# Optimization experiments

Hardware: AMD Instinct MI355X
Metric: run time of the kernel (lower is better)

Reference implementation:

```python
import jax, jax.numpy as jnp
import numpy as np

GAMMA = 10.0
EPS = 1e-6  # epsilon from __init__
B, D, C = 128, 1024, 1000


def setup_inputs() -> dict:
    key = jax.random.key(0)
    k1, k2, k3, k4 = jax.random.split(key, 4)
    return {
        "activations": jax.random.normal(k1, (B, D), jnp.float32),
        "W": jax.random.normal(k2, (D, C), jnp.float32) * 0.02,
        "b": jax.random.normal(k3, (C,), jnp.float32) * 0.02,
        "targets": jax.random.randint(k4, (B,), 0, C),
    }


def reference(activations, W, b, targets):
    # Linear classifier head: logits must be a differentiable fn of activations
    def head(a):  # [D] -> [C]
        return a @ W + b

    logits = jax.vmap(head)(activations)          # [B, C]
    # Batched Jacobian replaces the per-(i,j) torch.autograd.grad loop.
    J = jax.vmap(jax.jacrev(head))(activations)   # [B, C, D]

    t1h = jax.nn.one_hot(targets, C, dtype=logits.dtype)       # [B, C]
    correct = jnp.sum(logits * t1h, axis=1)                    # [B]
    grad_correct = jnp.einsum('bcd,bc->bd', J, t1h)            # [B, D]

    grad_diff = J - grad_correct[:, None, :]                   # [B, C, D]
    # dual norm (l2): sqrt(sum sq + eps), then forward adds +eps again
    dual_norm = jnp.sqrt(jnp.sum(grad_diff * grad_diff, axis=2) + EPS) + EPS  # [B, C]

    score_diff = logits - correct[:, None]                     # [B, C]
    violation = jax.nn.relu(GAMMA + score_diff / dual_norm)    # [B, C]
    violation = violation * (1.0 - t1h)  # exclude target class (relu >= 0 so max unaffected)

    loss = jnp.max(violation, axis=1)  # aggregation = 'max' over incorrect classes
    return jnp.mean(loss)
```

## Files before the change

kernel.cpp:

```cpp
#include <hip/hip_runtime.h>
#include <math.h>

#define Bn 128
#define Dn 1024
#define Cn 1000
#define Cpad 1024
#define GAMMA 10.0f
#define EPSv 1e-6f

#define DCH 32
#define DSPAN (Dn / DCH)
#define BM 8
#define NBG (Bn / BM)


__global__ __launch_bounds__(256) void lm_partial(
    const float* __restrict__ A, const float* __restrict__ W,
    const int* __restrict__ tgt,
    float* __restrict__ lg, float* __restrict__ dt,
    float* __restrict__ nrm, float* __restrict__ out)
{
    const int tid = threadIdx.x;
    const int bg  = blockIdx.x;
    const int k   = blockIdx.y;
    if (bg == 0 && k == 0 && tid == 0) out[0] = 0.f;

    const int b0 = bg * BM;
    const int d0 = k * DSPAN;
    const int c0 = tid * 4;
    const bool valid = (c0 < Cn);
    const int c0m = valid ? c0 : 0;

    __shared__ float4 AsI[2][DSPAN];
    __shared__ float4 WtI[2][DSPAN];
    {
        const int i = tid & (DSPAN - 1);
        const int j = tid >> 5;
        ((float*)&AsI[j >> 2][i])[j & 3] = A[(b0 + j) * Dn + d0 + i];
        ((float*)&WtI[j >> 2][i])[j & 3] = W[(size_t)(d0 + i) * Cn + tgt[b0 + j]];
    }
    __syncthreads();

    float aL[BM][4], aD[BM][4], aN[4];
    #pragma unroll
    for (int e = 0; e < 4; ++e) {
        aN[e] = 0.f;
        #pragma unroll
        for (int j = 0; j < BM; ++j) { aL[j][e] = 0.f; aD[j][e] = 0.f; }
    }

    const float* Wp = W + (size_t)d0 * Cn + c0m;
    #pragma unroll 2
    for (int i = 0; i < DSPAN; ++i) {
        const float4 w   = *(const float4*)(Wp + (size_t)i * Cn);
        const float4 a40 = AsI[0][i];
        const float4 a41 = AsI[1][i];
        const float4 t40 = WtI[0][i];
        const float4 t41 = WtI[1][i];
        const float wv[4] = {w.x, w.y, w.z, w.w};
        const float av[8] = {a40.x, a40.y, a40.z, a40.w, a41.x, a41.y, a41.z, a41.w};
        const float tv[8] = {t40.x, t40.y, t40.z, t40.w, t41.x, t41.y, t41.z, t41.w};
        #pragma unroll
        for (int e = 0; e < 4; ++e) {
            aN[e] = fmaf(wv[e], wv[e], aN[e]);
            #pragma unroll
            for (int j = 0; j < BM; ++j) {
                aL[j][e] = fmaf(av[j], wv[e], aL[j][e]);
                aD[j][e] = fmaf(tv[j], wv[e], aD[j][e]);
            }
        }
    }

    if (valid) {
        #pragma unroll
        for (int j = 0; j < BM; ++j) {
            const size_t off = ((size_t)(k * Bn + b0 + j)) * Cpad + c0;
            *(float4*)&lg[off] = make_float4(aL[j][0], aL[j][1], aL[j][2], aL[j][3]);
            *(float4*)&dt[off] = make_float4(aD[j][0], aD[j][1], aD[j][2], aD[j][3]);
        }
        if (bg == 0)
            *(float4*)&nrm[(size_t)k * Cpad + c0] =
                make_float4(aN[0], aN[1], aN[2], aN[3]);
    }
}

__global__ __launch_bounds__(256) void lm_final(
    const float* __restrict__ lg, const float* __restrict__ dt,
    const float* __restrict__ nrm, const float* __restrict__ bias,
    const int* __restrict__ tgt, float* __restrict__ out)
{
    const int b = blockIdx.x;
    const int tid = threadIdx.x;
    const int t = tgt[b];

    __shared__ float s_cr, s_nt;
    if (tid < DCH) {
        float cr = lg[((size_t)(tid * Bn + b)) * Cpad + t];
        float nt = nrm[(size_t)tid * Cpad + t];
        #pragma unroll
        for (int off = 16; off; off >>= 1) {
            cr += __shfl_down(cr, off, 64);
            nt += __shfl_down(nt, off, 64);
        }
        if (tid == 0) { s_cr = cr + bias[t]; s_nt = nt; }
    }
    __syncthreads();

    float m = 0.f;
    if (tid < 250) {
        const int c0 = tid * 4;
        float L[4] = {0.f,0.f,0.f,0.f}, Dt[4] = {0.f,0.f,0.f,0.f}, Nr[4] = {0.f,0.f,0.f,0.f};
        #pragma unroll 8
        for (int k = 0; k < DCH; ++k) {
            const float4 l4 = *(const float4*)&lg[((size_t)(k * Bn + b)) * Cpad + c0];
            const float4 d4 = *(const float4*)&dt[((size_t)(k * Bn + b)) * Cpad + c0];
            const float4 n4 = *(const float4*)&nrm[(size_t)k * Cpad + c0];
            L[0] += l4.x; L[1] += l4.y; L[2] += l4.z; L[3] += l4.w;
            Dt[0] += d4.x; Dt[1] += d4.y; Dt[2] += d4.z; Dt[3] += d4.w;
            Nr[0] += n4.x; Nr[1] += n4.y; Nr[2] += n4.z; Nr[3] += n4.w;
        }
        const float4 bi = *(const float4*)&bias[c0];
        const float bv[4] = {bi.x, bi.y, bi.z, bi.w};
        const float cr = s_cr, nt = s_nt;
        #pragma unroll
        for (int e = 0; e < 4; ++e) {
            const int c = c0 + e;
            if (c != t) {
                float dist = fmaxf(Nr[e] + nt - 2.f * Dt[e], 0.f);
                float dn   = sqrtf(dist + EPSv) + EPSv;
                float v    = GAMMA + (L[e] + bv[e] - cr) / dn;
                m = fmaxf(m, v);
            }
        }
    }

    for (int off = 32; off; off >>= 1) m = fmaxf(m, __shfl_down(m, off, 64));
    __shared__ float sm[4];
    if ((tid & 63) == 0) sm[tid >> 6] = m;
    __syncthreads();
    if (tid == 0) {
        const float bm = fmaxf(fmaxf(sm[0], sm[1]), fmaxf(sm[2], sm[3]));
        atomicAdd(out, bm * (1.0f / (float)Bn));
    }
}

extern "C" void kernel_launch(void* const* d_in, const int* in_sizes, int n_in,
                              void* d_out, int out_size, void* d_ws, size_t ws_size,
                              hipStream_t stream) {
    const float* A    = (const float*)d_in[0];
    const float* W    = (const float*)d_in[1];
    const float* bias = (const float*)d_in[2];
    const int*   tgt  = (const int*)d_in[3];
    float* out = (float*)d_out;

    float* lg  = (float*)d_ws;
    float* dt  = lg + (size_t)DCH * Bn * Cpad;
    float* nrm = dt + (size_t)DCH * Bn * Cpad;

    lm_partial<<<dim3(NBG, DCH), dim3(256), 0, stream>>>(A, W, tgt, lg, dt, nrm, out);
    lm_final<<<dim3(Bn), dim3(256), 0, stream>>>(lg, dt, nrm, bias, tgt, out);
}
```

Measured before the change: 83.98 us.

## Rebalance split-K partial GEMM and split class reduction across blocks

Halves the D-chunk count and the batch rows per block in the partial kernel. The grid stays the same size, but each thread keeps fewer accumulators and each block writes half as many partial sums to workspace. The final reduction is split into four class-quarters per batch row. Per-row maxima are combined with an integer atomicMax on float bits (valid because the values are non-negative), and a third tiny kernel averages them into the output. The cost is an extra kernel launch, and W is re-read with less reuse across batch rows per load.

```diff
diff --git a/kernel.cpp b/kernel.cpp
--- a/kernel.cpp
+++ b/kernel.cpp
@@ -8,9 +8,9 @@
 #define GAMMA 10.0f
 #define EPSv 1e-6f
 
-#define DCH 32
+#define DCH 16
 #define DSPAN (Dn / DCH)
-#define BM 8
+#define BM 4
 #define NBG (Bn / BM)
 
 
@@ -18,12 +18,12 @@
     const float* __restrict__ A, const float* __restrict__ W,
     const int* __restrict__ tgt,
     float* __restrict__ lg, float* __restrict__ dt,
-    float* __restrict__ nrm, float* __restrict__ out)
+    float* __restrict__ nrm, int* __restrict__ vmax)
 {
     const int tid = threadIdx.x;
     const int bg  = blockIdx.x;
     const int k   = blockIdx.y;
-    if (bg == 0 && k == 0 && tid == 0) out[0] = 0.f;
+    if (bg == 0 && k == 0 && tid < Bn) vmax[tid] = 0;
 
     const int b0 = bg * BM;
     const int d0 = k * DSPAN;
@@ -31,13 +31,13 @@
     const bool valid = (c0 < Cn);
     const int c0m = valid ? c0 : 0;
 
-    __shared__ float4 AsI[2][DSPAN];
-    __shared__ float4 WtI[2][DSPAN];
+    __shared__ float4 As4[DSPAN];
+    __shared__ float4 Wt4[DSPAN];
     {
         const int i = tid & (DSPAN - 1);
-        const int j = tid >> 5;
-        ((float*)&AsI[j >> 2][i])[j & 3] = A[(b0 + j) * Dn + d0 + i];
-        ((float*)&WtI[j >> 2][i])[j & 3] = W[(size_t)(d0 + i) * Cn + tgt[b0 + j]];
+        const int j = tid >> 6;
+        ((float*)&As4[i])[j] = A[(b0 + j) * Dn + d0 + i];
+        ((float*)&Wt4[i])[j] = W[(size_t)(d0 + i) * Cn + tgt[b0 + j]];
     }
     __syncthreads();
 
@@ -50,16 +50,14 @@
     }
 
     const float* Wp = W + (size_t)d0 * Cn + c0m;
-    #pragma unroll 2
+    #pragma unroll 4
     for (int i = 0; i < DSPAN; ++i) {
-        const float4 w   = *(const float4*)(Wp + (size_t)i * Cn);
-        const float4 a40 = AsI[0][i];
-        const float4 a41 = AsI[1][i];
-        const float4 t40 = WtI[0][i];
-        const float4 t41 = WtI[1][i];
+        const float4 w  = *(const float4*)(Wp + (size_t)i * Cn);
+        const float4 a4 = As4[i];
+        const float4 t4 = Wt4[i];
         const float wv[4] = {w.x, w.y, w.z, w.w};
-        const float av[8] = {a40.x, a40.y, a40.z, a40.w, a41.x, a41.y, a41.z, a41.w};
-        const float tv[8] = {t40.x, t40.y, t40.z, t40.w, t41.x, t41.y, t41.z, t41.w};
+        const float av[4] = {a4.x, a4.y, a4.z, a4.w};
+        const float tv[4] = {t4.x, t4.y, t4.z, t4.w};
         #pragma unroll
         for (int e = 0; e < 4; ++e) {
             aN[e] = fmaf(wv[e], wv[e], aN[e]);
@@ -84,21 +82,22 @@
     }
 }
 
-__global__ __launch_bounds__(256) void lm_final(
+__global__ __launch_bounds__(256) void lm_vmax(
     const float* __restrict__ lg, const float* __restrict__ dt,
     const float* __restrict__ nrm, const float* __restrict__ bias,
-    const int* __restrict__ tgt, float* __restrict__ out)
+    const int* __restrict__ tgt, int* __restrict__ vmax)
 {
-    const int b = blockIdx.x;
+    const int b   = blockIdx.x;
+    const int q   = blockIdx.y;
     const int tid = threadIdx.x;
-    const int t = tgt[b];
+    const int t   = tgt[b];
 
     __shared__ float s_cr, s_nt;
     if (tid < DCH) {
         float cr = lg[((size_t)(tid * Bn + b)) * Cpad + t];
         float nt = nrm[(size_t)tid * Cpad + t];
         #pragma unroll
-        for (int off = 16; off; off >>= 1) {
+        for (int off = DCH / 2; off; off >>= 1) {
             cr += __shfl_down(cr, off, 64);
             nt += __shfl_down(nt, off, 64);
         }
@@ -108,40 +107,43 @@
 
     float m = 0.f;
     if (tid < 250) {
-        const int c0 = tid * 4;
-        float L[4] = {0.f,0.f,0.f,0.f}, Dt[4] = {0.f,0.f,0.f,0.f}, Nr[4] = {0.f,0.f,0.f,0.f};
-        #pragma unroll 8
+        const int c = q * 250 + tid;
+        float L = 0.f, Dt = 0.f, Nr = 0.f;
+        #pragma unroll
         for (int k = 0; k < DCH; ++k) {
-            const float4 l4 = *(const float4*)&lg[((size_t)(k * Bn + b)) * Cpad + c0];
-            const float4 d4 = *(const float4*)&dt[((size_t)(k * Bn + b)) * Cpad + c0];
-            const float4 n4 = *(const float4*)&nrm[(size_t)k * Cpad + c0];
-            L[0] += l4.x; L[1] += l4.y; L[2] += l4.z; L[3] += l4.w;
-            Dt[0] += d4.x; Dt[1] += d4.y; Dt[2] += d4.z; Dt[3] += d4.w;
-            Nr[0] += n4.x; Nr[1] += n4.y; Nr[2] += n4.z; Nr[3] += n4.w;
+            L  += lg[((size_t)(k * Bn + b)) * Cpad + c];
+            Dt += dt[((size_t)(k * Bn + b)) * Cpad + c];
+            Nr += nrm[(size_t)k * Cpad + c];
         }
-        const float4 bi = *(const float4*)&bias[c0];
-        const float bv[4] = {bi.x, bi.y, bi.z, bi.w};
-        const float cr = s_cr, nt = s_nt;
-        #pragma unroll
-        for (int e = 0; e < 4; ++e) {
-            const int c = c0 + e;
-            if (c != t) {
-                float dist = fmaxf(Nr[e] + nt - 2.f * Dt[e], 0.f);
-                float dn   = sqrtf(dist + EPSv) + EPSv;
-                float v    = GAMMA + (L[e] + bv[e] - cr) / dn;
-                m = fmaxf(m, v);
-            }
+        if (c != t) {
+            const float dist = fmaxf(Nr + s_nt - 2.f * Dt, 0.f);
+            const float dn   = sqrtf(dist + EPSv) + EPSv;
+            m = fmaxf(0.f, GAMMA + (L + bias[c] - s_cr) / dn);
         }
     }
 
+    #pragma unroll
     for (int off = 32; off; off >>= 1) m = fmaxf(m, __shfl_down(m, off, 64));
     __shared__ float sm[4];
     if ((tid & 63) == 0) sm[tid >> 6] = m;
     __syncthreads();
     if (tid == 0) {
         const float bm = fmaxf(fmaxf(sm[0], sm[1]), fmaxf(sm[2], sm[3]));
-        atomicAdd(out, bm * (1.0f / (float)Bn));
+        atomicMax(vmax + b, __float_as_int(bm));
     }
+}
+
+__global__ __launch_bounds__(128) void lm_mean(
+    const int* __restrict__ vmax, float* __restrict__ out)
+{
+    const int tid = threadIdx.x;
+    float v = __int_as_float(vmax[tid]);
+    #pragma unroll
+    for (int off = 32; off; off >>= 1) v += __shfl_down(v, off, 64);
+    __shared__ float sw[2];
+    if ((tid & 63) == 0) sw[tid >> 6] = v;
+    __syncthreads();
+    if (tid == 0) out[0] = (sw[0] + sw[1]) * (1.0f / (float)Bn);
 }
 
 extern "C" void kernel_launch(void* const* d_in, const int* in_sizes, int n_in,
@@ -156,7 +158,9 @@
     float* lg  = (float*)d_ws;
     float* dt  = lg + (size_t)DCH * Bn * Cpad;
     float* nrm = dt + (size_t)DCH * Bn * Cpad;
+    int*   vmx = (int*)(nrm + (size_t)DCH * Cpad);
 
-    lm_partial<<<dim3(NBG, DCH), dim3(256), 0, stream>>>(A, W, tgt, lg, dt, nrm, out);
-    lm_final<<<dim3(Bn), dim3(256), 0, stream>>>(lg, dt, nrm, bias, tgt, out);
+    lm_partial<<<dim3(NBG, DCH), dim3(256), 0, stream>>>(A, W, tgt, lg, dt, nrm, vmx);
+    lm_vmax  <<<dim3(Bn, 4),    dim3(256), 0, stream>>>(lg, dt, nrm, bias, tgt, vmx);
+    lm_mean  <<<dim3(1),        dim3(128), 0, stream>>>(vmx, out);
 }
```

Measured after the change: 84.26 us. About the same (+0.3%).
